# Performance work log

Hardware: AMD Instinct MI355X
Metric: run time of the kernel (lower is better)

The kernel has to match this reference:

```python
import jax, jax.numpy as jnp
import numpy as np

W_BITS = 4  # active precision (max of supported_bits)
EPS = 0.005  # clamp margin from the original module


def _dequant_kbit(qweight, lut, w_bits):
    """Bit-plane LUT dequant.
    qweight: [w_bits, O, I//32] int32, plane b holds bit b (MSB-first code) of each
    weight's k-bit index, 32 consecutive input positions per int32 word (LSB-first
    within a word). lut: [O, 2**w_bits]. Returns dense weight [O, I].
    """
    O = qweight.shape[1]
    shifts = jnp.arange(32, dtype=jnp.int32)                     # bit position within word
    bits = (qweight[:, :, :, None] >> shifts) & 1                # [w_bits, O, I//32, 32]
    plane_w = (1 << (w_bits - 1 - jnp.arange(w_bits, dtype=jnp.int32)))
    idx = (bits * plane_w[:, None, None, None]).sum(axis=0)      # [O, I//32, 32]
    idx = idx.reshape(O, -1)                                     # [O, I]
    return jnp.take_along_axis(lut, idx, axis=1)                 # [O, I]


def _csr_dense(rows, cols, vals, O, I):
    """Scatter CSR (indptr=rows) into a dense [O, I] matrix."""
    nnz = cols.shape[0]
    k = jnp.arange(nnz, dtype=rows.dtype)
    row_ids = jnp.searchsorted(rows, k, side='right') - 1        # CSR row of each nnz
    return jnp.zeros((O, I), dtype=vals.dtype).at[row_ids, cols].add(vals)


def setup_inputs() -> dict:
    key = jax.random.key(0)
    ks = jax.random.split(key, 7)
    B, S, I, O = 4, 2048, 4096, 4096
    NNZ = 65536
    x = jax.random.normal(ks[0], (B, S, I), dtype=jnp.float32)
    qweight = jax.random.randint(ks[1], (W_BITS, O, I // 32), 0, 2147483647, dtype=jnp.int32)
    lut = jax.random.normal(ks[2], (O, 2 ** W_BITS), dtype=jnp.float32) * 0.05
    rows = jnp.sort(jax.random.randint(ks[3], (O + 1,), 0, NNZ, dtype=jnp.int32))
    rows = rows.at[0].set(0).at[-1].set(NNZ)                     # valid CSR indptr
    cols = jax.random.randint(ks[4], (NNZ,), 0, I, dtype=jnp.int32)
    vals = jax.random.normal(ks[5], (NNZ,), dtype=jnp.float32) * 0.01
    bias = jax.random.normal(ks[6], (O,), dtype=jnp.float32) * 0.01
    return {"x": x, "qweight": qweight, "lut": lut, "rows": rows,
            "cols": cols, "vals": vals, "bias": bias}


def reference(x, qweight, lut, rows, cols, vals, bias):
    O = qweight.shape[1]
    I = x.shape[-1]
    weight = _dequant_kbit(qweight, lut, W_BITS)                 # [O, I]
    y = jnp.einsum('bsi,oi->bso', x, weight)                     # dense quantized GEMM
    w_sp = _csr_dense(rows, cols, vals, O, I)                    # sparse outlier weights
    y = y + jnp.einsum('bsi,oi->bso', x, w_sp)
    y = y + bias
    fmax = jnp.finfo(x.dtype).max * (1.0 - EPS)
    return jnp.clip(y, -fmax, fmax)
```

## Files before the change

kernel.cpp:

```cpp
#include <hip/hip_runtime.h>
#include <stdint.h>

#define Mdim 8192
#define Ndim 4096
#define Kdim 4096

#define BM 256
#define BN 256
#define BK 64
#define NT2 (Kdim / BK)

typedef float f32x4 __attribute__((ext_vector_type(4)));
typedef __bf16 bf16x8 __attribute__((ext_vector_type(8)));
typedef unsigned short ushort_t;

#define FMAXC 3.3858093490333422e+38f

__device__ __forceinline__ ushort_t f2bf(float f) {
    unsigned u = __float_as_uint(f);
    u += 0x7fffu + ((u >> 16) & 1u);
    return (ushort_t)(u >> 16);
}

__device__ __forceinline__ void gload_lds16(const void* g, void* l) {
    __builtin_amdgcn_global_load_lds(
        (const __attribute__((address_space(1))) uint32_t*)g,
        (__attribute__((address_space(3))) uint32_t*)(uint32_t)(uintptr_t)l,
        16, 0, 0);
}

#define SGB(mask, n) __builtin_amdgcn_sched_group_barrier(mask, n, 0)

__global__ __launch_bounds__(128) void dequant_kernel(
        const int* __restrict__ qw, const float* __restrict__ lut,
        const int* __restrict__ rows, const int* __restrict__ cols,
        const float* __restrict__ vals, ushort_t* __restrict__ w16) {
    __shared__ float wrow[128 * 33];
    __shared__ float slut[16];
    const int o = blockIdx.x;
    const int t = threadIdx.x;

    if (t < 16) slut[t] = lut[o * 16 + t];
    __syncthreads();

    const int q0 = qw[0 * Ndim * 128 + o * 128 + t];
    const int q1 = qw[1 * Ndim * 128 + o * 128 + t];
    const int q2 = qw[2 * Ndim * 128 + o * 128 + t];
    const int q3 = qw[3 * Ndim * 128 + o * 128 + t];
    float* dst = &wrow[t * 33];
#pragma unroll
    for (int j = 0; j < 32; ++j) {
        int idx = (((q0 >> j) & 1) << 3) | (((q1 >> j) & 1) << 2) |
                  (((q2 >> j) & 1) << 1) | ((q3 >> j) & 1);
        dst[j] = slut[idx];
    }
    __syncthreads();

    const int beg = rows[o], end = rows[o + 1];
    for (int k = beg + t; k < end; k += 128) {
        int c = cols[k];
        atomicAdd(&wrow[c + (c >> 5)], vals[k]);
    }
    __syncthreads();

    __align__(16) ushort_t tmp[32];
#pragma unroll
    for (int j = 0; j < 32; ++j) tmp[j] = f2bf(dst[j]);
    uint4* dstg = (uint4*)(w16 + (size_t)o * Kdim + t * 32);
    const uint4* srcg = (const uint4*)tmp;
#pragma unroll
    for (int j = 0; j < 4; ++j) dstg[j] = srcg[j];
}

__global__ __launch_bounds__(256) void convx_kernel(
        const float* __restrict__ x, ushort_t* __restrict__ y) {
    size_t i = ((size_t)blockIdx.x * 256 + threadIdx.x) * 8;
    float4 a = *(const float4*)(x + i);
    float4 b = *(const float4*)(x + i + 4);
    __align__(16) ushort_t r[8] = {f2bf(a.x), f2bf(a.y), f2bf(a.z), f2bf(a.w),
                                   f2bf(b.x), f2bf(b.y), f2bf(b.z), f2bf(b.w)};
    *(uint4*)(y + i) = *(const uint4*)r;
}

__global__ __launch_bounds__(512, 2) void gemm_kernel(
        const ushort_t* __restrict__ A, const ushort_t* __restrict__ Bw,
        const float* __restrict__ bias, float* __restrict__ C) {
    __shared__ __align__(16) char lds[131072];

    const int wgid = blockIdx.x;
    const int swz = (wgid & 7) * 64 + (wgid >> 3);
    const int bn = swz & 15, bm = swz >> 4;
    const int m0 = bm * BM, n0 = bn * BN;

    const int tid = threadIdx.x;
    const int lane = tid & 63, wid = tid >> 6;
    const int wr = wid >> 2, wc = wid & 3;
    const int fr = lane & 15, kg = lane >> 4;

    const int srow = tid >> 3;
    const int scol = (((tid & 7) ^ (srow & 7)) * 8);
    const ushort_t* gA = A + (size_t)(m0 + srow) * Kdim + scol;
    const ushort_t* gB = Bw + (size_t)(n0 + srow) * Kdim + scol;

    const int off0 = fr * 128 + (((kg) ^ (fr & 7)) << 4);
    const int off1 = fr * 128 + (((4 | kg) ^ (fr & 7)) << 4);

    f32x4 acc[8][4];
#pragma unroll
    for (int i = 0; i < 8; ++i)
#pragma unroll
        for (int j = 0; j < 4; ++j) acc[i][j] = (f32x4){0.f, 0.f, 0.f, 0.f};

    auto stage = [&](int buf, int t1) {
        const ushort_t* sa = gA + (size_t)t1 * BK;
        const ushort_t* sb = gB + (size_t)t1 * BK;
        char* da = lds + buf * 65536 + tid * 16;
        char* db = da + 32768;
#pragma unroll
        for (int j = 0; j < 4; ++j) {
            gload_lds16(sa + (size_t)j * 64 * Kdim, da + j * 8192);
            gload_lds16(sb + (size_t)j * 64 * Kdim, db + j * 8192);
        }
    };
    auto readA = [&](bf16x8 (&FA)[8], const char* Ab, int off) {
#pragma unroll
        for (int m = 0; m < 8; ++m)
            FA[m] = *(const bf16x8*)(Ab + wr * 16384 + m * 2048 + off);
    };
    auto readB = [&](bf16x8 (&FB)[4], const char* Bb, int off) {
#pragma unroll
        for (int n = 0; n < 4; ++n)
            FB[n] = *(const bf16x8*)(Bb + wc * 8192 + n * 2048 + off);
    };
    auto mfmaK = [&](bf16x8 (&FA)[8], bf16x8 (&FB)[4]) {
#pragma unroll
        for (int m = 0; m < 8; ++m)
#pragma unroll
            for (int n = 0; n < 4; ++n)
                acc[m][n] = __builtin_amdgcn_mfma_f32_16x16x32_bf16(
                    FA[m], FB[n], acc[m][n], 0, 0, 0);
    };

    stage(0, 0);
    asm volatile("s_waitcnt vmcnt(0)");
    __builtin_amdgcn_sched_barrier(0);
    __builtin_amdgcn_s_barrier();

#pragma unroll 1
    for (int t = 0; t < NT2 - 1; ++t) {
        const char* Ab = lds + (t & 1) * 65536;
        const char* Bb = Ab + 32768;

        bf16x8 A0[8], B0[4], A1[8], B1[4];
        readA(A0, Ab, off0); readB(B0, Bb, off0);
        stage((t + 1) & 1, t + 1);
        readA(A1, Ab, off1); readB(B1, Bb, off1);

        __builtin_amdgcn_s_setprio(1);
        mfmaK(A0, B0);
        mfmaK(A1, B1);
        __builtin_amdgcn_s_setprio(0);

        SGB(0x100, 12);
#pragma unroll
        for (int i = 0; i < 4; ++i) { SGB(0x30, 2); SGB(0x8, 4); }
#pragma unroll
        for (int i = 0; i < 6; ++i) { SGB(0x100, 2); SGB(0x8, 2); }
        SGB(0x8, 36);

        asm volatile("s_waitcnt vmcnt(0)");
        __builtin_amdgcn_sched_barrier(0);
        __builtin_amdgcn_s_barrier();
    }

    {
        const char* Ab = lds + ((NT2 - 1) & 1) * 65536;
        const char* Bb = Ab + 32768;
        bf16x8 A0[8], B0[4], A1[8], B1[4];
        readA(A0, Ab, off0); readB(B0, Bb, off0);
        readA(A1, Ab, off1); readB(B1, Bb, off1);
        mfmaK(A0, B0);
        mfmaK(A1, B1);
    }

    const int rg = lane >> 4;
#pragma unroll
    for (int nf = 0; nf < 4; ++nf) {
        const int col = n0 + wc * 64 + nf * 16 + fr;
        const float bv = bias[col];
#pragma unroll
        for (int mf = 0; mf < 8; ++mf) {
            const int row = m0 + wr * 128 + mf * 16 + rg * 4;
            float* outp = C + (size_t)row * Ndim + col;
#pragma unroll
            for (int j = 0; j < 4; ++j) {
                float v = acc[mf][nf][j] + bv;
                v = fminf(fmaxf(v, -FMAXC), FMAXC);
                outp[(size_t)j * Ndim] = v;
            }
        }
    }
}

extern "C" void kernel_launch(void* const* d_in, const int* in_sizes, int n_in,
                              void* d_out, int out_size, void* d_ws, size_t ws_size,
                              hipStream_t stream) {
    const float* x    = (const float*)d_in[0];
    const int*   qw   = (const int*)d_in[1];
    const float* lut  = (const float*)d_in[2];
    const int*   rows = (const int*)d_in[3];
    const int*   cols = (const int*)d_in[4];
    const float* vals = (const float*)d_in[5];
    const float* bias = (const float*)d_in[6];
    float* out = (float*)d_out;

    ushort_t* x16 = (ushort_t*)d_ws;
    ushort_t* w16 = x16 + (size_t)Mdim * Kdim;

    hipLaunchKernelGGL(dequant_kernel, dim3(Ndim), dim3(128), 0, stream,
                       qw, lut, rows, cols, vals, w16);
    hipLaunchKernelGGL(convx_kernel, dim3((Mdim * Kdim) / (256 * 8)), dim3(256), 0, stream,
                       x, x16);
    hipLaunchKernelGGL(gemm_kernel, dim3((Mdim / BM) * (Ndim / BN)), dim3(512), 0, stream,
                       x16, w16, bias, out);
}
```

Baseline: 275.7 us.

## Load B fragments directly from global into registers, halving LDS use

The GEMM no longer stages the weight tile through LDS. Each wave loads its B fragments straight from global memory into registers, prefetched one k-step ahead, and only the A tile stays double-buffered in LDS (64KB instead of 128KB). The goal is to cut LDS traffic and footprint, and to make room for more resident workgroups. The cost is that each B fragment is now fetched separately by the wr=0 and wr=1 wave rows, and B reads are narrow 16-byte per-lane global loads. The waitcnt and scheduling-barrier pattern is reworked to keep those B loads in flight across barriers.

```diff
diff --git a/kernel.cpp b/kernel.cpp
--- a/kernel.cpp
+++ b/kernel.cpp
@@ -85,7 +85,7 @@
 __global__ __launch_bounds__(512, 2) void gemm_kernel(
         const ushort_t* __restrict__ A, const ushort_t* __restrict__ Bw,
         const float* __restrict__ bias, float* __restrict__ C) {
-    __shared__ __align__(16) char lds[131072];
+    __shared__ __align__(16) char lds[65536];
 
     const int wgid = blockIdx.x;
     const int swz = (wgid & 7) * 64 + (wgid >> 3);
@@ -100,87 +100,120 @@
     const int srow = tid >> 3;
     const int scol = (((tid & 7) ^ (srow & 7)) * 8);
     const ushort_t* gA = A + (size_t)(m0 + srow) * Kdim + scol;
-    const ushort_t* gB = Bw + (size_t)(n0 + srow) * Kdim + scol;
 
     const int off0 = fr * 128 + (((kg) ^ (fr & 7)) << 4);
     const int off1 = fr * 128 + (((4 | kg) ^ (fr & 7)) << 4);
 
+    const ushort_t* pB0 = Bw + (size_t)(n0 + wc * 64 + 0 * 16 + fr) * Kdim + kg * 8;
+    const ushort_t* pB1 = pB0 + (size_t)16 * Kdim;
+    const ushort_t* pB2 = pB0 + (size_t)32 * Kdim;
+    const ushort_t* pB3 = pB0 + (size_t)48 * Kdim;
+
     f32x4 acc[8][4];
 #pragma unroll
     for (int i = 0; i < 8; ++i)
 #pragma unroll
         for (int j = 0; j < 4; ++j) acc[i][j] = (f32x4){0.f, 0.f, 0.f, 0.f};
 
-    auto stage = [&](int buf, int t1) {
-        const ushort_t* sa = gA + (size_t)t1 * BK;
-        const ushort_t* sb = gB + (size_t)t1 * BK;
-        char* da = lds + buf * 65536 + tid * 16;
-        char* db = da + 32768;
-#pragma unroll
-        for (int j = 0; j < 4; ++j) {
-            gload_lds16(sa + (size_t)j * 64 * Kdim, da + j * 8192);
-            gload_lds16(sb + (size_t)j * 64 * Kdim, db + j * 8192);
-        }
+    const ushort_t* pAs = gA;
+    auto stageA = [&](int buf) {
+        char* d = lds + buf * 32768 + tid * 16;
+#pragma unroll
+        for (int j = 0; j < 4; ++j)
+            gload_lds16(pAs + (size_t)j * 64 * Kdim, d + j * 8192);
     };
-    auto readA = [&](bf16x8 (&FA)[8], const char* Ab, int off) {
-#pragma unroll
-        for (int m = 0; m < 8; ++m)
-            FA[m] = *(const bf16x8*)(Ab + wr * 16384 + m * 2048 + off);
+
+    auto halfTile = [&](int bufi, int bufn, bf16x8 (&Bc)[4], bf16x8 (&Bn)[4]) {
+        const char* Ab = lds + bufi * 32768;
+        stageA(bufn);
+        pAs += BK;
+
+        bf16x8 FA0[8];
+#pragma unroll
+        for (int m = 0; m < 8; ++m)
+            FA0[m] = *(const bf16x8*)(Ab + wr * 16384 + m * 2048 + off0);
+        bf16x8 Bt[4];
+        Bt[0] = *(const bf16x8*)(pB0 + 32); Bt[1] = *(const bf16x8*)(pB1 + 32);
+        Bt[2] = *(const bf16x8*)(pB2 + 32); Bt[3] = *(const bf16x8*)(pB3 + 32);
+
+        __builtin_amdgcn_s_setprio(1);
+#pragma unroll
+        for (int m = 0; m < 8; ++m)
+#pragma unroll
+            for (int n = 0; n < 4; ++n)
+                acc[m][n] = __builtin_amdgcn_mfma_f32_16x16x32_bf16(
+                    FA0[m], Bc[n], acc[m][n], 0, 0, 0);
+
+        bf16x8 FA1[8];
+#pragma unroll
+        for (int m = 0; m < 8; ++m)
+            FA1[m] = *(const bf16x8*)(Ab + wr * 16384 + m * 2048 + off1);
+        Bn[0] = *(const bf16x8*)(pB0 + 64); Bn[1] = *(const bf16x8*)(pB1 + 64);
+        Bn[2] = *(const bf16x8*)(pB2 + 64); Bn[3] = *(const bf16x8*)(pB3 + 64);
+
+#pragma unroll
+        for (int m = 0; m < 8; ++m)
+#pragma unroll
+            for (int n = 0; n < 4; ++n)
+                acc[m][n] = __builtin_amdgcn_mfma_f32_16x16x32_bf16(
+                    FA1[m], Bt[n], acc[m][n], 0, 0, 0);
+        __builtin_amdgcn_s_setprio(0);
+        pB0 += BK; pB1 += BK; pB2 += BK; pB3 += BK;
+
+        SGB(0x30, 4);
+        SGB(0x100, 2); SGB(0x30, 4);
+#pragma unroll
+        for (int i = 0; i < 6; ++i) { SGB(0x8, 4); SGB(0x100, 1); }
+        SGB(0x8, 8);
+        SGB(0x100, 2); SGB(0x30, 4);
+#pragma unroll
+        for (int i = 0; i < 6; ++i) { SGB(0x8, 4); SGB(0x100, 1); }
+        SGB(0x8, 8);
+
+        asm volatile("s_waitcnt vmcnt(4)");
+        __builtin_amdgcn_sched_barrier(0);
+        __builtin_amdgcn_s_barrier();
     };
-    auto readB = [&](bf16x8 (&FB)[4], const char* Bb, int off) {
-#pragma unroll
-        for (int n = 0; n < 4; ++n)
-            FB[n] = *(const bf16x8*)(Bb + wc * 8192 + n * 2048 + off);
-    };
-    auto mfmaK = [&](bf16x8 (&FA)[8], bf16x8 (&FB)[4]) {
-#pragma unroll
-        for (int m = 0; m < 8; ++m)
-#pragma unroll
-            for (int n = 0; n < 4; ++n)
-                acc[m][n] = __builtin_amdgcn_mfma_f32_16x16x32_bf16(
-                    FA[m], FB[n], acc[m][n], 0, 0, 0);
-    };
-
-    stage(0, 0);
-    asm volatile("s_waitcnt vmcnt(0)");
+
+    bf16x8 BA[4], BB[4];
+    stageA(0);
+    pAs += BK;
+    BA[0] = *(const bf16x8*)(pB0); BA[1] = *(const bf16x8*)(pB1);
+    BA[2] = *(const bf16x8*)(pB2); BA[3] = *(const bf16x8*)(pB3);
+    asm volatile("s_waitcnt vmcnt(4)");
     __builtin_amdgcn_sched_barrier(0);
     __builtin_amdgcn_s_barrier();
 
 #pragma unroll 1
-    for (int t = 0; t < NT2 - 1; ++t) {
-        const char* Ab = lds + (t & 1) * 65536;
-        const char* Bb = Ab + 32768;
-
-        bf16x8 A0[8], B0[4], A1[8], B1[4];
-        readA(A0, Ab, off0); readB(B0, Bb, off0);
-        stage((t + 1) & 1, t + 1);
-        readA(A1, Ab, off1); readB(B1, Bb, off1);
-
-        __builtin_amdgcn_s_setprio(1);
-        mfmaK(A0, B0);
-        mfmaK(A1, B1);
-        __builtin_amdgcn_s_setprio(0);
-
-        SGB(0x100, 12);
-#pragma unroll
-        for (int i = 0; i < 4; ++i) { SGB(0x30, 2); SGB(0x8, 4); }
-#pragma unroll
-        for (int i = 0; i < 6; ++i) { SGB(0x100, 2); SGB(0x8, 2); }
-        SGB(0x8, 36);
-
-        asm volatile("s_waitcnt vmcnt(0)");
-        __builtin_amdgcn_sched_barrier(0);
-        __builtin_amdgcn_s_barrier();
-    }
+    for (int t = 0; t < NT2 - 2; t += 2) {
+        halfTile(0, 1, BA, BB);
+        halfTile(1, 0, BB, BA);
+    }
+    halfTile(0, 1, BA, BB);
 
     {
-        const char* Ab = lds + ((NT2 - 1) & 1) * 65536;
-        const char* Bb = Ab + 32768;
-        bf16x8 A0[8], B0[4], A1[8], B1[4];
-        readA(A0, Ab, off0); readB(B0, Bb, off0);
-        readA(A1, Ab, off1); readB(B1, Bb, off1);
-        mfmaK(A0, B0);
-        mfmaK(A1, B1);
+        const char* Ab = lds + 32768;
+        bf16x8 FA0[8], FA1[8], Bt[4];
+#pragma unroll
+        for (int m = 0; m < 8; ++m)
+            FA0[m] = *(const bf16x8*)(Ab + wr * 16384 + m * 2048 + off0);
+        Bt[0] = *(const bf16x8*)(pB0 + 32); Bt[1] = *(const bf16x8*)(pB1 + 32);
+        Bt[2] = *(const bf16x8*)(pB2 + 32); Bt[3] = *(const bf16x8*)(pB3 + 32);
+#pragma unroll
+        for (int m = 0; m < 8; ++m)
+#pragma unroll
+            for (int n = 0; n < 4; ++n)
+                acc[m][n] = __builtin_amdgcn_mfma_f32_16x16x32_bf16(
+                    FA0[m], BB[n], acc[m][n], 0, 0, 0);
+#pragma unroll
+        for (int m = 0; m < 8; ++m)
+            FA1[m] = *(const bf16x8*)(Ab + wr * 16384 + m * 2048 + off1);
+#pragma unroll
+        for (int m = 0; m < 8; ++m)
+#pragma unroll
+            for (int n = 0; n < 4; ++n)
+                acc[m][n] = __builtin_amdgcn_mfma_f32_16x16x32_bf16(
+                    FA1[m], Bt[n], acc[m][n], 0, 0, 0);
     }
 
     const int rg = lane >> 4;
```

Result: slower. 345.6 us (+25.4%).

## Shrink GEMM tile to 256x128x32 with smaller LDS for higher occupancy

Applied to the files above, without the earlier changes.

Reduces the GEMM block tile from 256x256 with BK=64 to 256x128 with BK=32. The LDS buffer drops from 128KB to 48KB, the per-wave accumulator from 8x4 to 4x4 fragments, and the launch bound asks for 4 blocks per CU. The LDS swizzle layout, wave decomposition, grid swizzle and schedule-group hints are reworked to match. More resident waves should hide latency better, at the cost of less data reuse per tile and twice as many K iterations, each with its own barrier.

```diff
diff --git a/kernel.cpp b/kernel.cpp
--- a/kernel.cpp
+++ b/kernel.cpp
@@ -6,9 +6,9 @@
 #define Kdim 4096
 
 #define BM 256
-#define BN 256
-#define BK 64
-#define NT2 (Kdim / BK)
+#define BN 128
+#define BK 32
+#define NT (Kdim / BK)
 
 typedef float f32x4 __attribute__((ext_vector_type(4)));
 typedef __bf16 bf16x8 __attribute__((ext_vector_type(8)));
@@ -82,63 +82,43 @@
     *(uint4*)(y + i) = *(const uint4*)r;
 }
 
-__global__ __launch_bounds__(512, 2) void gemm_kernel(
+__global__ __launch_bounds__(512, 4) void gemm_kernel(
         const ushort_t* __restrict__ A, const ushort_t* __restrict__ Bw,
         const float* __restrict__ bias, float* __restrict__ C) {
-    __shared__ __align__(16) char lds[131072];
+    __shared__ __align__(16) char lds[49152];
 
     const int wgid = blockIdx.x;
-    const int swz = (wgid & 7) * 64 + (wgid >> 3);
-    const int bn = swz & 15, bm = swz >> 4;
+    const int swz = (wgid & 7) * 128 + (wgid >> 3);
+    const int bn = swz & 31, bm = swz >> 5;
     const int m0 = bm * BM, n0 = bn * BN;
 
     const int tid = threadIdx.x;
     const int lane = tid & 63, wid = tid >> 6;
-    const int wr = wid >> 2, wc = wid & 3;
+    const int wr = wid >> 1, wc = wid & 1;
     const int fr = lane & 15, kg = lane >> 4;
 
-    const int srow = tid >> 3;
-    const int scol = (((tid & 7) ^ (srow & 7)) * 8);
-    const ushort_t* gA = A + (size_t)(m0 + srow) * Kdim + scol;
-    const ushort_t* gB = Bw + (size_t)(n0 + srow) * Kdim + scol;
-
-    const int off0 = fr * 128 + (((kg) ^ (fr & 7)) << 4);
-    const int off1 = fr * 128 + (((4 | kg) ^ (fr & 7)) << 4);
-
-    f32x4 acc[8][4];
-#pragma unroll
-    for (int i = 0; i < 8; ++i)
+    const int sline = tid >> 3;
+    const int slot = (tid & 7) ^ (sline & 7);
+    const int srow0 = (sline << 1) + (slot >> 2);
+    const int skel = (slot & 3) * 8;
+    const ushort_t* gA = A + (size_t)(m0 + srow0) * Kdim + skel;
+    const ushort_t* gB = Bw + (size_t)(n0 + srow0) * Kdim + skel;
+
+    const int offL = (fr >> 1) * 128 + (((((fr & 1) << 2) | kg) ^ (fr >> 1)) << 4);
+
+    f32x4 acc[4][4];
+#pragma unroll
+    for (int i = 0; i < 4; ++i)
 #pragma unroll
         for (int j = 0; j < 4; ++j) acc[i][j] = (f32x4){0.f, 0.f, 0.f, 0.f};
 
     auto stage = [&](int buf, int t1) {
         const ushort_t* sa = gA + (size_t)t1 * BK;
         const ushort_t* sb = gB + (size_t)t1 * BK;
-        char* da = lds + buf * 65536 + tid * 16;
-        char* db = da + 32768;
-#pragma unroll
-        for (int j = 0; j < 4; ++j) {
-            gload_lds16(sa + (size_t)j * 64 * Kdim, da + j * 8192);
-            gload_lds16(sb + (size_t)j * 64 * Kdim, db + j * 8192);
-        }
-    };
-    auto readA = [&](bf16x8 (&FA)[8], const char* Ab, int off) {
-#pragma unroll
-        for (int m = 0; m < 8; ++m)
-            FA[m] = *(const bf16x8*)(Ab + wr * 16384 + m * 2048 + off);
-    };
-    auto readB = [&](bf16x8 (&FB)[4], const char* Bb, int off) {
-#pragma unroll
-        for (int n = 0; n < 4; ++n)
-            FB[n] = *(const bf16x8*)(Bb + wc * 8192 + n * 2048 + off);
-    };
-    auto mfmaK = [&](bf16x8 (&FA)[8], bf16x8 (&FB)[4]) {
-#pragma unroll
-        for (int m = 0; m < 8; ++m)
-#pragma unroll
-            for (int n = 0; n < 4; ++n)
-                acc[m][n] = __builtin_amdgcn_mfma_f32_16x16x32_bf16(
-                    FA[m], FB[n], acc[m][n], 0, 0, 0);
+        char* d = lds + buf * 24576 + tid * 16;
+        gload_lds16(sa, d);
+        gload_lds16(sa + (size_t)128 * Kdim, d + 8192);
+        gload_lds16(sb, d + 16384);
     };
 
     stage(0, 0);
@@ -147,26 +127,32 @@
     __builtin_amdgcn_s_barrier();
 
 #pragma unroll 1
-    for (int t = 0; t < NT2 - 1; ++t) {
-        const char* Ab = lds + (t & 1) * 65536;
-        const char* Bb = Ab + 32768;
-
-        bf16x8 A0[8], B0[4], A1[8], B1[4];
-        readA(A0, Ab, off0); readB(B0, Bb, off0);
+    for (int t = 0; t < NT - 1; ++t) {
+        const char* Ab = lds + (t & 1) * 24576;
+        const char* Bb = Ab + 16384;
+
         stage((t + 1) & 1, t + 1);
-        readA(A1, Ab, off1); readB(B1, Bb, off1);
+
+        bf16x8 FA[4], FB[4];
+#pragma unroll
+        for (int m = 0; m < 4; ++m)
+            FA[m] = *(const bf16x8*)(Ab + wr * 4096 + m * 1024 + offL);
+#pragma unroll
+        for (int n = 0; n < 4; ++n)
+            FB[n] = *(const bf16x8*)(Bb + wc * 4096 + n * 1024 + offL);
 
         __builtin_amdgcn_s_setprio(1);
-        mfmaK(A0, B0);
-        mfmaK(A1, B1);
+#pragma unroll
+        for (int m = 0; m < 4; ++m)
+#pragma unroll
+            for (int n = 0; n < 4; ++n)
+                acc[m][n] = __builtin_amdgcn_mfma_f32_16x16x32_bf16(
+                    FA[m], FB[n], acc[m][n], 0, 0, 0);
         __builtin_amdgcn_s_setprio(0);
 
-        SGB(0x100, 12);
-#pragma unroll
-        for (int i = 0; i < 4; ++i) { SGB(0x30, 2); SGB(0x8, 4); }
-#pragma unroll
-        for (int i = 0; i < 6; ++i) { SGB(0x100, 2); SGB(0x8, 2); }
-        SGB(0x8, 36);
+        SGB(0x30, 3);
+        SGB(0x100, 8);
+        SGB(0x8, 16);
 
         asm volatile("s_waitcnt vmcnt(0)");
         __builtin_amdgcn_sched_barrier(0);
@@ -174,13 +160,21 @@
     }
 
     {
-        const char* Ab = lds + ((NT2 - 1) & 1) * 65536;
-        const char* Bb = Ab + 32768;
-        bf16x8 A0[8], B0[4], A1[8], B1[4];
-        readA(A0, Ab, off0); readB(B0, Bb, off0);
-        readA(A1, Ab, off1); readB(B1, Bb, off1);
-        mfmaK(A0, B0);
-        mfmaK(A1, B1);
+        const char* Ab = lds + ((NT - 1) & 1) * 24576;
+        const char* Bb = Ab + 16384;
+        bf16x8 FA[4], FB[4];
+#pragma unroll
+        for (int m = 0; m < 4; ++m)
+            FA[m] = *(const bf16x8*)(Ab + wr * 4096 + m * 1024 + offL);
+#pragma unroll
+        for (int n = 0; n < 4; ++n)
+            FB[n] = *(const bf16x8*)(Bb + wc * 4096 + n * 1024 + offL);
+#pragma unroll
+        for (int m = 0; m < 4; ++m)
+#pragma unroll
+            for (int n = 0; n < 4; ++n)
+                acc[m][n] = __builtin_amdgcn_mfma_f32_16x16x32_bf16(
+                    FA[m], FB[n], acc[m][n], 0, 0, 0);
     }
 
     const int rg = lane >> 4;
@@ -189,8 +183,8 @@
         const int col = n0 + wc * 64 + nf * 16 + fr;
         const float bv = bias[col];
 #pragma unroll
-        for (int mf = 0; mf < 8; ++mf) {
-            const int row = m0 + wr * 128 + mf * 16 + rg * 4;
+        for (int mf = 0; mf < 4; ++mf) {
+            const int row = m0 + wr * 64 + mf * 16 + rg * 4;
             float* outp = C + (size_t)row * Ndim + col;
 #pragma unroll
             for (int j = 0; j < 4; ++j) {
```

Result: slower. 321.4 us (+16.6%).

## Switch GEMM inner tile to 32x32x16 bf16 MFMA with restructured fragments

Applied to the files above, without the earlier changes.

Replaces the 16x16x32 MFMA tiling (8x4 fragments per wave) with 32x32x16 MFMA instructions (4x2 fragments of 16-wide accumulators). LDS fragment offsets, the fragment reads, the sched_group_barrier interleaving and the epilogue row mapping are rebuilt to match the new layout. The larger MFMA shape is meant to cut LDS read traffic per FLOP and the instruction count. In exchange it changes register pressure and the LDS bank access pattern.

```diff
diff --git a/kernel.cpp b/kernel.cpp
--- a/kernel.cpp
+++ b/kernel.cpp
@@ -11,6 +11,7 @@
 #define NT2 (Kdim / BK)
 
 typedef float f32x4 __attribute__((ext_vector_type(4)));
+typedef float f32x16 __attribute__((ext_vector_type(16)));
 typedef __bf16 bf16x8 __attribute__((ext_vector_type(8)));
 typedef unsigned short ushort_t;
 
@@ -95,21 +96,25 @@
     const int tid = threadIdx.x;
     const int lane = tid & 63, wid = tid >> 6;
     const int wr = wid >> 2, wc = wid & 3;
-    const int fr = lane & 15, kg = lane >> 4;
+    const int l31 = lane & 31, kg2 = lane >> 5;
 
     const int srow = tid >> 3;
     const int scol = (((tid & 7) ^ (srow & 7)) * 8);
     const ushort_t* gA = A + (size_t)(m0 + srow) * Kdim + scol;
     const ushort_t* gB = Bw + (size_t)(n0 + srow) * Kdim + scol;
 
-    const int off0 = fr * 128 + (((kg) ^ (fr & 7)) << 4);
-    const int off1 = fr * 128 + (((4 | kg) ^ (fr & 7)) << 4);
-
-    f32x4 acc[8][4];
-#pragma unroll
-    for (int i = 0; i < 8; ++i)
-#pragma unroll
-        for (int j = 0; j < 4; ++j) acc[i][j] = (f32x4){0.f, 0.f, 0.f, 0.f};
+    int offK[4];
+#pragma unroll
+    for (int ks = 0; ks < 4; ++ks)
+        offK[ks] = l31 * 128 + ((((ks << 1) | kg2) ^ (lane & 7)) << 4);
+
+    f32x16 acc[4][2];
+#pragma unroll
+    for (int i = 0; i < 4; ++i)
+#pragma unroll
+        for (int j = 0; j < 2; ++j)
+#pragma unroll
+            for (int e = 0; e < 16; ++e) acc[i][j][e] = 0.f;
 
     auto stage = [&](int buf, int t1) {
         const ushort_t* sa = gA + (size_t)t1 * BK;
@@ -122,23 +127,30 @@
             gload_lds16(sb + (size_t)j * 64 * Kdim, db + j * 8192);
         }
     };
-    auto readA = [&](bf16x8 (&FA)[8], const char* Ab, int off) {
-#pragma unroll
-        for (int m = 0; m < 8; ++m)
-            FA[m] = *(const bf16x8*)(Ab + wr * 16384 + m * 2048 + off);
+    auto readFrags = [&](bf16x8 (&FA)[4][4], bf16x8 (&FB)[2][4], const char* Ab,
+                         const char* Bb) {
+#pragma unroll
+        for (int mf = 0; mf < 4; ++mf)
+#pragma unroll
+            for (int ks = 0; ks < 4; ++ks)
+                FA[mf][ks] = *(const bf16x8*)(Ab + wr * 16384 + mf * 4096 + offK[ks]);
+#pragma unroll
+        for (int nf = 0; nf < 2; ++nf)
+#pragma unroll
+            for (int ks = 0; ks < 4; ++ks)
+                FB[nf][ks] = *(const bf16x8*)(Bb + wc * 8192 + nf * 4096 + offK[ks]);
     };
-    auto readB = [&](bf16x8 (&FB)[4], const char* Bb, int off) {
-#pragma unroll
-        for (int n = 0; n < 4; ++n)
-            FB[n] = *(const bf16x8*)(Bb + wc * 8192 + n * 2048 + off);
-    };
-    auto mfmaK = [&](bf16x8 (&FA)[8], bf16x8 (&FB)[4]) {
-#pragma unroll
-        for (int m = 0; m < 8; ++m)
-#pragma unroll
-            for (int n = 0; n < 4; ++n)
-                acc[m][n] = __builtin_amdgcn_mfma_f32_16x16x32_bf16(
-                    FA[m], FB[n], acc[m][n], 0, 0, 0);
+    auto mfmaTile = [&](bf16x8 (&FA)[4][4], bf16x8 (&FB)[2][4]) {
+        __builtin_amdgcn_s_setprio(1);
+#pragma unroll
+        for (int ks = 0; ks < 4; ++ks)
+#pragma unroll
+            for (int mf = 0; mf < 4; ++mf)
+#pragma unroll
+                for (int nf = 0; nf < 2; ++nf)
+                    acc[mf][nf] = __builtin_amdgcn_mfma_f32_32x32x16_bf16(
+                        FA[mf][ks], FB[nf][ks], acc[mf][nf], 0, 0, 0);
+        __builtin_amdgcn_s_setprio(0);
     };
 
     stage(0, 0);
@@ -151,22 +163,14 @@
         const char* Ab = lds + (t & 1) * 65536;
         const char* Bb = Ab + 32768;
 
-        bf16x8 A0[8], B0[4], A1[8], B1[4];
-        readA(A0, Ab, off0); readB(B0, Bb, off0);
+        bf16x8 FA[4][4], FB[2][4];
+        readFrags(FA, FB, Ab, Bb);
         stage((t + 1) & 1, t + 1);
-        readA(A1, Ab, off1); readB(B1, Bb, off1);
-
-        __builtin_amdgcn_s_setprio(1);
-        mfmaK(A0, B0);
-        mfmaK(A1, B1);
-        __builtin_amdgcn_s_setprio(0);
-
-        SGB(0x100, 12);
-#pragma unroll
-        for (int i = 0; i < 4; ++i) { SGB(0x30, 2); SGB(0x8, 4); }
-#pragma unroll
-        for (int i = 0; i < 6; ++i) { SGB(0x100, 2); SGB(0x8, 2); }
-        SGB(0x8, 36);
+        mfmaTile(FA, FB);
+
+        SGB(0x30, 8);
+#pragma unroll
+        for (int i = 0; i < 8; ++i) { SGB(0x100, 3); SGB(0x8, 4); }
 
         asm volatile("s_waitcnt vmcnt(0)");
         __builtin_amdgcn_sched_barrier(0);
@@ -176,27 +180,24 @@
     {
         const char* Ab = lds + ((NT2 - 1) & 1) * 65536;
         const char* Bb = Ab + 32768;
-        bf16x8 A0[8], B0[4], A1[8], B1[4];
-        readA(A0, Ab, off0); readB(B0, Bb, off0);
-        readA(A1, Ab, off1); readB(B1, Bb, off1);
-        mfmaK(A0, B0);
-        mfmaK(A1, B1);
-    }
-
-    const int rg = lane >> 4;
-#pragma unroll
-    for (int nf = 0; nf < 4; ++nf) {
-        const int col = n0 + wc * 64 + nf * 16 + fr;
+        bf16x8 FA[4][4], FB[2][4];
+        readFrags(FA, FB, Ab, Bb);
+        mfmaTile(FA, FB);
+    }
+
+#pragma unroll
+    for (int nf = 0; nf < 2; ++nf) {
+        const int col = n0 + wc * 64 + nf * 32 + l31;
         const float bv = bias[col];
 #pragma unroll
-        for (int mf = 0; mf < 8; ++mf) {
-            const int row = m0 + wr * 128 + mf * 16 + rg * 4;
-            float* outp = C + (size_t)row * Ndim + col;
-#pragma unroll
-            for (int j = 0; j < 4; ++j) {
-                float v = acc[mf][nf][j] + bv;
+        for (int mf = 0; mf < 4; ++mf) {
+            const int rowbase = m0 + wr * 128 + mf * 32 + 4 * kg2;
+#pragma unroll
+            for (int r = 0; r < 16; ++r) {
+                const int row = rowbase + (r & 3) + 8 * (r >> 2);
+                float v = acc[mf][nf][r] + bv;
                 v = fminf(fmaxf(v, -FMAXC), FMAXC);
-                outp[(size_t)j * Ndim] = v;
+                C[(size_t)row * Ndim + col] = v;
             }
         }
     }
```

Measured after the change: 302.0 us. 1.1x slower.
